# Optimization experiments

Measured on AMD Instinct MI355X. Metric: run time of the kernel, lower is better.

Reference implementation:

```python
import jax, jax.numpy as jnp
import numpy as np


def setup_inputs() -> dict:
    key = jax.random.key(0)
    kx, ks = jax.random.split(key)
    X = jax.random.normal(kx, (8, 4096, 16), dtype=jnp.float32)
    # nn.Parameter(torch.rand(1) + 1.0)
    sigma = jax.random.uniform(ks, (1,), dtype=jnp.float32) + 1.0
    return {"X": X, "sigma": sigma}


def reference(X, sigma):
    sq = jnp.sum(X * X, axis=-1)                       # [B, N]
    inner = jnp.einsum('bnf,bmf->bnm', X, X)           # [B, N, N]
    sqdist = sq[:, :, None] + sq[:, None, :] - 2.0 * inner
    sqdist = jnp.maximum(sqdist, 0.0)                  # guard tiny negatives
    gaussian = jnp.exp(-sqdist / sigma[0])             # [B, N, N]
    # original _softmax: exp(gaussian) / sum over dim 2 == softmax over axis 2
    return jax.nn.softmax(gaussian, axis=2)
```

## Files before the change

### kernel.cpp

```cpp
#include <hip/hip_runtime.h>


typedef float v4f __attribute__((ext_vector_type(4)));
typedef short bf8 __attribute__((ext_vector_type(8)));

constexpr int Bn  = 8;
constexpr int N   = 4096;
constexpr int F   = 16;
constexpr int BM  = 16;
constexpr int BLK = 1024;
constexpr int NW  = BLK / 64;
constexpr int TPW = (N / 16) / NW;
constexpr int ROWB = N * 2 + 8;

__device__ __forceinline__ unsigned short f2bf(float x) {
    unsigned int u = __float_as_uint(x);
    unsigned int r = (u + 0x7FFFu + ((u >> 16) & 1u)) >> 16;
    return (unsigned short)r;
}
__device__ __forceinline__ float bf2f(unsigned short h) {
    return __uint_as_float(((unsigned int)h) << 16);
}
__device__ __forceinline__ float uni(float x) {
    return __int_as_float(__builtin_amdgcn_readfirstlane(__float_as_int(x)));
}

__global__ __launch_bounds__(256)
void pack_kernel(const float* __restrict__ X, uint4* __restrict__ Xp,
                 float* __restrict__ sqm) {
    const int b = blockIdx.y;
    const int m = blockIdx.x * 256 + threadIdx.x;
    const float4* src = (const float4*)(X + ((size_t)b * N + m) * F);
    const float4 v0 = src[0], v1 = src[1], v2 = src[2], v3 = src[3];
    const float x[F] = {v0.x, v0.y, v0.z, v0.w, v1.x, v1.y, v1.z, v1.w,
                        v2.x, v2.y, v2.z, v2.w, v3.x, v3.y, v3.z, v3.w};
    float s = 0.f;
    #pragma unroll
    for (int f = 0; f < F; ++f) s = fmaf(x[f], x[f], s);
    sqm[(size_t)b * N + m] = s;

    uint4* dst = Xp + ((size_t)b * N + m) * 4;
    #pragma unroll
    for (int g = 0; g < 4; ++g) {
        unsigned int hi[4], lo[4];
        #pragma unroll
        for (int j = 0; j < 4; ++j) {
            const float xf = x[4 * g + j];
            const unsigned short h = f2bf(xf);
            hi[j] = h;
            lo[j] = f2bf(xf - bf2f(h));
        }
        uint4 c;
        c.x = hi[0] | (hi[1] << 16);
        c.y = hi[2] | (hi[3] << 16);
        c.z = lo[0] | (lo[1] << 16);
        c.w = lo[2] | (lo[3] << 16);
        dst[g] = c;
    }
}

union BfU { uint4 u; bf8 h; };

__global__ __launch_bounds__(BLK)
void gs_mfma(const uint4* __restrict__ Xp, const float* __restrict__ sqm,
             const float* __restrict__ sigma_p, float* __restrict__ out) {
    extern __shared__ char smem[];
    float* red = (float*)(smem + (size_t)BM * ROWB);

    const int tid  = threadIdx.x;
    const int w    = tid >> 6;
    const int lane = tid & 63;
    const int g    = lane >> 4;
    const int c    = lane & 15;
    const int b    = blockIdx.y;
    const int n0   = blockIdx.x * BM;

    const uint4* Xpb = Xp + (size_t)b * N * 4;
    const float* sqb = sqm + (size_t)b * N;

    BfU b1; b1.u = Xpb[(size_t)(n0 + c) * 4 + g];
    BfU b2; b2.u = make_uint4(b1.u.z, b1.u.w, b1.u.x, b1.u.y);

    const float sqn_l = sqb[n0 + c];
    const float nis   = uni(-1.0f / sigma_p[0]);

    float psum = 0.f;

    #pragma unroll
    for (int t = 0; t < TPW; ++t) {
        const int m_tile = w * (TPW * 16) + t * 16;
        BfU a; a.u = Xpb[(size_t)(m_tile + c) * 4 + g];

        v4f acc = {0.f, 0.f, 0.f, 0.f};
        acc = __builtin_amdgcn_mfma_f32_16x16x32_bf16(a.h, b1.h, acc, 0, 0, 0);
        acc = __builtin_amdgcn_mfma_f32_16x16x32_bf16(a.h, b2.h, acc, 0, 0, 0);

        const v4f sm4 = *(const v4f*)(sqb + m_tile + 4 * g);
        float ex = __expf(__expf(fmaxf(fmaf(-2.f, acc.x, sqn_l + sm4.x), 0.f) * nis));
        float ey = __expf(__expf(fmaxf(fmaf(-2.f, acc.y, sqn_l + sm4.y), 0.f) * nis));
        float ez = __expf(__expf(fmaxf(fmaf(-2.f, acc.z, sqn_l + sm4.z), 0.f) * nis));
        float ew = __expf(__expf(fmaxf(fmaf(-2.f, acc.w, sqn_l + sm4.w), 0.f) * nis));

        ushort4 pk;
        pk.x = f2bf(ex); pk.y = f2bf(ey); pk.z = f2bf(ez); pk.w = f2bf(ew);
        const int gl = (m_tile >> 2) + g;
        *(ushort4*)(smem + (size_t)c * ROWB + 8 * gl) = pk;

        psum += (ex + ey) + (ez + ew);
    }

    psum += __shfl_xor(psum, 16, 64);
    psum += __shfl_xor(psum, 32, 64);
    if (lane < 16) red[w * BM + lane] = psum;
    __syncthreads();

    float tot = 0.f;
    #pragma unroll
    for (int w2 = 0; w2 < NW; ++w2) tot += red[w2 * BM + w];
    const float inv = uni(1.0f / tot);

    float* rowp = out + ((size_t)b * N + n0 + w) * (size_t)N;
    #pragma unroll
    for (int k = 0; k < N / 4 / 64; ++k) {
        const int gp = 64 * k + lane;
        const ushort4 pk = *(const ushort4*)(smem + (size_t)w * ROWB + 8 * gp);
        v4f v;
        v.x = bf2f(pk.x) * inv;
        v.y = bf2f(pk.y) * inv;
        v.z = bf2f(pk.z) * inv;
        v.w = bf2f(pk.w) * inv;
        __builtin_nontemporal_store(v, (v4f*)rowp + gp);
    }
}

extern "C" void kernel_launch(void* const* d_in, const int* in_sizes, int n_in,
                              void* d_out, int out_size, void* d_ws, size_t ws_size,
                              hipStream_t stream) {
    const float* X     = (const float*)d_in[0];
    const float* sigma = (const float*)d_in[1];
    float* out         = (float*)d_out;
    uint4* Xp          = (uint4*)d_ws;
    float* sqm         = (float*)d_ws + (size_t)Bn * N * 16;

    const size_t lds_bytes = (size_t)BM * ROWB + NW * BM * 4;
    pack_kernel<<<dim3(N / 256, Bn), 256, 0, stream>>>(X, Xp, sqm);
    gs_mfma<<<dim3(N / BM, Bn), BLK, lds_bytes, stream>>>(Xp, sqm, sigma, out);
}
```

Baseline: 558.1 us.

## Keep exp results in registers and stage output through small chunked LDS buffer

Halves the block to 512 threads and keeps the bf16-packed exp values in registers instead of a full 16x4096 LDS row buffer. Output is then written in four 1024-column chunks through a much smaller LDS staging area, so more blocks can reside per CU. Stores change from nontemporal to regular, and the row normalizer is computed once by one wave. The trade-off is higher register pressure (64 packed words per thread) and extra barriers per chunk.

```diff
diff --git a/kernel.cpp b/kernel.cpp
--- a/kernel.cpp
+++ b/kernel.cpp
@@ -8,10 +8,11 @@
 constexpr int N   = 4096;
 constexpr int F   = 16;
 constexpr int BM  = 16;
-constexpr int BLK = 1024;
+constexpr int BLK = 512;
 constexpr int NW  = BLK / 64;
-constexpr int TPW = (N / 16) / NW;
-constexpr int ROWB = N * 2 + 8;
+constexpr int NCH = 4;
+constexpr int TPC = 8;
+constexpr int ROWC = 1024 * 2 + 8;
 
 __device__ __forceinline__ unsigned short f2bf(float x) {
     unsigned int u = __float_as_uint(x);
@@ -61,75 +62,98 @@
 
 union BfU { uint4 u; bf8 h; };
 
-__global__ __launch_bounds__(BLK)
+__global__ __launch_bounds__(BLK, 4)
 void gs_mfma(const uint4* __restrict__ Xp, const float* __restrict__ sqm,
              const float* __restrict__ sigma_p, float* __restrict__ out) {
     extern __shared__ char smem[];
-    float* red = (float*)(smem + (size_t)BM * ROWB);
+    float* red   = (float*)(smem + (size_t)BM * ROWC);
+    float* inv16 = red + NW * BM;
 
     const int tid  = threadIdx.x;
     const int w    = tid >> 6;
     const int lane = tid & 63;
     const int g    = lane >> 4;
-    const int c    = lane & 15;
+    const int cc   = lane & 15;
     const int b    = blockIdx.y;
     const int n0   = blockIdx.x * BM;
 
     const uint4* Xpb = Xp + (size_t)b * N * 4;
     const float* sqb = sqm + (size_t)b * N;
 
-    BfU b1; b1.u = Xpb[(size_t)(n0 + c) * 4 + g];
+    BfU b1; b1.u = Xpb[(size_t)(n0 + cc) * 4 + g];
     BfU b2; b2.u = make_uint4(b1.u.z, b1.u.w, b1.u.x, b1.u.y);
 
-    const float sqn_l = sqb[n0 + c];
+    const float sqn_l = sqb[n0 + cc];
     const float nis   = uni(-1.0f / sigma_p[0]);
 
+    unsigned int e_pk[NCH * TPC * 2];
     float psum = 0.f;
 
     #pragma unroll
-    for (int t = 0; t < TPW; ++t) {
-        const int m_tile = w * (TPW * 16) + t * 16;
-        BfU a; a.u = Xpb[(size_t)(m_tile + c) * 4 + g];
+    for (int c = 0; c < NCH; ++c) {
+        #pragma unroll
+        for (int t = 0; t < TPC; ++t) {
+            const int m_tile = (c * 64 + w * TPC + t) * 16;
+            BfU a; a.u = Xpb[(size_t)(m_tile + cc) * 4 + g];
 
-        v4f acc = {0.f, 0.f, 0.f, 0.f};
-        acc = __builtin_amdgcn_mfma_f32_16x16x32_bf16(a.h, b1.h, acc, 0, 0, 0);
-        acc = __builtin_amdgcn_mfma_f32_16x16x32_bf16(a.h, b2.h, acc, 0, 0, 0);
+            v4f acc = {0.f, 0.f, 0.f, 0.f};
+            acc = __builtin_amdgcn_mfma_f32_16x16x32_bf16(a.h, b1.h, acc, 0, 0, 0);
+            acc = __builtin_amdgcn_mfma_f32_16x16x32_bf16(a.h, b2.h, acc, 0, 0, 0);
 
-        const v4f sm4 = *(const v4f*)(sqb + m_tile + 4 * g);
-        float ex = __expf(__expf(fmaxf(fmaf(-2.f, acc.x, sqn_l + sm4.x), 0.f) * nis));
-        float ey = __expf(__expf(fmaxf(fmaf(-2.f, acc.y, sqn_l + sm4.y), 0.f) * nis));
-        float ez = __expf(__expf(fmaxf(fmaf(-2.f, acc.z, sqn_l + sm4.z), 0.f) * nis));
-        float ew = __expf(__expf(fmaxf(fmaf(-2.f, acc.w, sqn_l + sm4.w), 0.f) * nis));
+            const v4f sm4 = *(const v4f*)(sqb + m_tile + 4 * g);
+            float ex = __expf(__expf(fmaxf(fmaf(-2.f, acc.x, sqn_l + sm4.x), 0.f) * nis));
+            float ey = __expf(__expf(fmaxf(fmaf(-2.f, acc.y, sqn_l + sm4.y), 0.f) * nis));
+            float ez = __expf(__expf(fmaxf(fmaf(-2.f, acc.z, sqn_l + sm4.z), 0.f) * nis));
+            float ew = __expf(__expf(fmaxf(fmaf(-2.f, acc.w, sqn_l + sm4.w), 0.f) * nis));
 
-        ushort4 pk;
-        pk.x = f2bf(ex); pk.y = f2bf(ey); pk.z = f2bf(ez); pk.w = f2bf(ew);
-        const int gl = (m_tile >> 2) + g;
-        *(ushort4*)(smem + (size_t)c * ROWB + 8 * gl) = pk;
-
-        psum += (ex + ey) + (ez + ew);
+            e_pk[(c * TPC + t) * 2 + 0] = (unsigned int)f2bf(ex) | ((unsigned int)f2bf(ey) << 16);
+            e_pk[(c * TPC + t) * 2 + 1] = (unsigned int)f2bf(ez) | ((unsigned int)f2bf(ew) << 16);
+            psum += (ex + ey) + (ez + ew);
+        }
     }
 
     psum += __shfl_xor(psum, 16, 64);
     psum += __shfl_xor(psum, 32, 64);
     if (lane < 16) red[w * BM + lane] = psum;
     __syncthreads();
+    if (w == 0 && lane < 16) {
+        float tot = 0.f;
+        #pragma unroll
+        for (int w2 = 0; w2 < NW; ++w2) tot += red[w2 * BM + lane];
+        inv16[lane] = 1.0f / tot;
+    }
+    __syncthreads();
 
-    float tot = 0.f;
     #pragma unroll
-    for (int w2 = 0; w2 < NW; ++w2) tot += red[w2 * BM + w];
-    const float inv = uni(1.0f / tot);
+    for (int c = 0; c < NCH; ++c) {
+        #pragma unroll
+        for (int t = 0; t < TPC; ++t) {
+            const int gl = (w * TPC + t) * 4 + g;
+            uint2 pk;
+            pk.x = e_pk[(c * TPC + t) * 2 + 0];
+            pk.y = e_pk[(c * TPC + t) * 2 + 1];
+            *(uint2*)(smem + (size_t)cc * ROWC + 8 * gl) = pk;
+        }
+        __syncthreads();
 
-    float* rowp = out + ((size_t)b * N + n0 + w) * (size_t)N;
-    #pragma unroll
-    for (int k = 0; k < N / 4 / 64; ++k) {
-        const int gp = 64 * k + lane;
-        const ushort4 pk = *(const ushort4*)(smem + (size_t)w * ROWB + 8 * gp);
-        v4f v;
-        v.x = bf2f(pk.x) * inv;
-        v.y = bf2f(pk.y) * inv;
-        v.z = bf2f(pk.z) * inv;
-        v.w = bf2f(pk.w) * inv;
-        __builtin_nontemporal_store(v, (v4f*)rowp + gp);
+        #pragma unroll
+        for (int rsel = 0; rsel < 2; ++rsel) {
+            const int rr = w + rsel * NW;
+            const float invr = inv16[rr];
+            float* rowp = out + ((size_t)b * N + n0 + rr) * (size_t)N + c * 1024;
+            #pragma unroll
+            for (int k = 0; k < 4; ++k) {
+                const int gp = 64 * k + lane;
+                const uint2 pk = *(const uint2*)(smem + (size_t)rr * ROWC + 8 * gp);
+                v4f v;
+                v.x = __uint_as_float(pk.x << 16) * invr;
+                v.y = __uint_as_float(pk.x & 0xffff0000u) * invr;
+                v.z = __uint_as_float(pk.y << 16) * invr;
+                v.w = __uint_as_float(pk.y & 0xffff0000u) * invr;
+                ((v4f*)rowp)[gp] = v;
+            }
+        }
+        __syncthreads();
     }
 }
 
@@ -142,7 +166,7 @@
     uint4* Xp          = (uint4*)d_ws;
     float* sqm         = (float*)d_ws + (size_t)Bn * N * 16;
 
-    const size_t lds_bytes = (size_t)BM * ROWB + NW * BM * 4;
+    const size_t lds_bytes = (size_t)BM * ROWC + NW * BM * 4 + 16 * 4;
     pack_kernel<<<dim3(N / 256, Bn), 256, 0, stream>>>(X, Xp, sqm);
     gs_mfma<<<dim3(N / BM, Bn), BLK, lds_bytes, stream>>>(Xp, sqm, sigma, out);
 }
```

Measured after the change: 591.0 us. 1.06x slower.
